# Performance work log

Measured on AMD Instinct MI355X. Metric: run time of the kernel, lower is better.

Reference implementation:

```python
import jax, jax.numpy as jnp
import numpy as np

D_MODEL = 768
N_HEADS = 12
D_K = D_MODEL // N_HEADS
B, S = 2, 2048
EPS = 1e-5  # torch LayerNorm default


def setup_inputs() -> dict:
    key = jax.random.key(0)
    ks = jax.random.split(key, 12)
    sc = 1.0 / np.sqrt(D_MODEL)
    inp = {
        "q": jax.random.normal(ks[0], (B, S, D_MODEL), jnp.float32),
        "k": jax.random.normal(ks[1], (B, S, D_MODEL), jnp.float32),
        "v": jax.random.normal(ks[2], (B, S, D_MODEL), jnp.float32),
        # causal mask: 1 = keep, 0 = masked
        "mask": jnp.tril(jnp.ones((S, S), jnp.int32))[None, None, :, :],
        "Wq": jax.random.normal(ks[3], (D_MODEL, D_MODEL), jnp.float32) * sc,
        "bq": jnp.zeros((D_MODEL,), jnp.float32),
        "Wk": jax.random.normal(ks[4], (D_MODEL, D_MODEL), jnp.float32) * sc,
        "bk": jnp.zeros((D_MODEL,), jnp.float32),
        "Wv": jax.random.normal(ks[5], (D_MODEL, D_MODEL), jnp.float32) * sc,
        "bv": jnp.zeros((D_MODEL,), jnp.float32),
        "Wo": jax.random.normal(ks[6], (D_MODEL, D_MODEL), jnp.float32) * sc,
        "bo": jnp.zeros((D_MODEL,), jnp.float32),
        "gamma": jnp.ones((D_MODEL,), jnp.float32),
        "beta": jnp.zeros((D_MODEL,), jnp.float32),
    }
    return inp


def _layernorm(x, gamma, beta):
    mu = jnp.mean(x, axis=-1, keepdims=True)
    var = jnp.mean(jnp.square(x - mu), axis=-1, keepdims=True)
    return (x - mu) * jax.lax.rsqrt(var + EPS) * gamma + beta


def reference(q, k, v, mask, Wq, bq, Wk, bk, Wv, bv, Wo, bo, gamma, beta):
    residual = q
    # projections + split heads: [B,S,D] -> [B,H,S,Dk]
    def split_heads(x):
        return x.reshape(B, S, N_HEADS, D_K).transpose(0, 2, 1, 3)
    Q = split_heads(q @ Wq.T + bq)
    K = split_heads(k @ Wk.T + bk)
    V = split_heads(v @ Wv.T + bv)
    scores = jnp.einsum("bhqd,bhkd->bhqk", Q, K) / jnp.sqrt(jnp.float32(D_K))
    scores = jnp.where(mask == 0, -jnp.inf, scores)
    attn = jax.nn.softmax(scores, axis=-1)
    # dropout is identity in eval mode
    out = jnp.einsum("bhqk,bhkd->bhqd", attn, V)
    out = out.transpose(0, 2, 1, 3).reshape(B, S, D_MODEL)
    out = out @ Wo.T + bo
    out = _layernorm(residual + out, gamma, beta)
    return (out, attn)
```

## Files before the change

kernel.cpp:

```cpp
#include <hip/hip_runtime.h>
#include <math.h>

typedef __attribute__((ext_vector_type(8))) short bf8_t;
typedef __attribute__((ext_vector_type(4))) float f4_t;

#define MFMA(a,b,c) __builtin_amdgcn_mfma_f32_16x16x32_bf16(a,b,c,0,0,0)

static constexpr int S_ = 2048;
static constexpr size_t QKV_ELEMS = 3145728;
static constexpr size_t W_ELEMS   = 589824;
static constexpr size_t OUT0_ELEMS = 3145728;

__device__ __forceinline__ unsigned short f2bf(float f) {
    union { float f; unsigned u; } v; v.f = f;
    unsigned u = v.u;
    u += 0x7fffu + ((u >> 16) & 1u);
    return (unsigned short)(u >> 16);
}

__device__ __forceinline__ void gload_lds16(const short* g, short* l) {
    __builtin_amdgcn_global_load_lds((const __attribute__((address_space(1))) void*)g,
                                     (__attribute__((address_space(3))) void*)l,
                                     16, 0, 0);
}

struct CvtP { const float* s[7]; unsigned short* d[7]; int n[7]; };

__global__ __launch_bounds__(256)
void cvt_all(CvtP p)
{
    const int z = blockIdx.z;
    const int i = (blockIdx.x * 256 + threadIdx.x) * 8;
    if (i >= p.n[z]) return;
    const float* s = p.s[z] + i;
    float4 a = *(const float4*)s, b = *(const float4*)(s + 4);
    uint4 u;
    u.x = (unsigned)f2bf(a.x) | ((unsigned)f2bf(a.y) << 16);
    u.y = (unsigned)f2bf(a.z) | ((unsigned)f2bf(a.w) << 16);
    u.z = (unsigned)f2bf(b.x) | ((unsigned)f2bf(b.y) << 16);
    u.w = (unsigned)f2bf(b.z) | ((unsigned)f2bf(b.w) << 16);
    *(uint4*)(p.d[z] + i) = u;
}

struct GemmP {
    const short* A[3]; const short* W[3]; const float* bias[3];
    void* C[3]; float scale[3]; int mode[3];
};

__global__ __launch_bounds__(256)
void gemm_bf16(GemmP p)
{
    const int z = blockIdx.z;
    const short* __restrict__ A = p.A[z];
    const short* __restrict__ W = p.W[z];
    const float* __restrict__ bias = p.bias[z];
    const float scale = p.scale[z];
    const int mode = p.mode[z];

    __shared__ short As[128 * 32];
    __shared__ short Bs[128 * 32];

    const int t = threadIdx.x;
    const int m0 = blockIdx.y * 128, n0 = blockIdx.x * 128;
    const int w = t >> 6, lane = t & 63, li = lane & 15, qd = lane >> 4;
    const int wm = (w & 1) * 64, wn = (w >> 1) * 64;

    f4_t acc[4][4];
    #pragma unroll
    for (int i = 0; i < 4; ++i)
        #pragma unroll
        for (int j = 0; j < 4; ++j)
            #pragma unroll
            for (int r = 0; r < 4; ++r) acc[i][j][r] = 0.f;

    for (int k0 = 0; k0 < 768; k0 += 32) {
        #pragma unroll
        for (int e = 0; e < 2; ++e) {
            const int ch = t + e * 256;
            const int r = ch >> 2, c = (ch & 3) << 3;
            gload_lds16(&A[(size_t)(m0 + r) * 768 + k0 + c], &As[ch << 3]);
            gload_lds16(&W[(size_t)(n0 + r) * 768 + k0 + c], &Bs[ch << 3]);
        }
        __syncthreads();
        bf8_t af[4], bf[4];
        #pragma unroll
        for (int i = 0; i < 4; ++i) af[i] = *(const bf8_t*)&As[(wm + i * 16 + li) * 32 + qd * 8];
        #pragma unroll
        for (int j = 0; j < 4; ++j) bf[j] = *(const bf8_t*)&Bs[(wn + j * 16 + li) * 32 + qd * 8];
        #pragma unroll
        for (int i = 0; i < 4; ++i)
            #pragma unroll
            for (int j = 0; j < 4; ++j)
                acc[i][j] = MFMA(af[i], bf[j], acc[i][j]);
        __syncthreads();
    }

    #pragma unroll
    for (int i = 0; i < 4; ++i) {
        const int row = m0 + wm + i * 16 + qd * 4;
        #pragma unroll
        for (int j = 0; j < 4; ++j) {
            const int col = n0 + wn + j * 16 + li;
            const float bv = bias[col];
            float vals[4];
            #pragma unroll
            for (int r = 0; r < 4; ++r) vals[r] = (acc[i][j][r] + bv) * scale;
            if (mode == 0) {
                const int head = col >> 6;
                const int cq = col & 63;
                const int half = cq >> 5, qd_ = (cq >> 3) & 3, e = cq & 7;
                #pragma unroll
                for (int r = 0; r < 4; ++r) {
                    const int rr = row + r;
                    const int bh = (rr >> 11) * 12 + head;
                    const int s = rr & 2047;
                    const int kt = s >> 6, sub = (s >> 4) & 3, li_ = s & 15;
                    const size_t idx = ((((size_t)bh * 32 + kt) * 2 + half) * 4 + sub) * 512
                                     + li_ * 32 + qd_ * 8 + e;
                    ((unsigned short*)p.C[z])[idx] = f2bf(vals[r]);
                }
            } else if (mode == 1) {
                const int head = col >> 6;
                const int rr = row;
                const int bh = (rr >> 11) * 12 + head;
                const int s = rr & 2047;
                const int kt = s >> 6, h = (s >> 5) & 1, qd_ = (s >> 3) & 3, e0 = s & 7;
                const int d_ = (col & 63) >> 4, li_ = col & 15;
                const size_t idx = (((((size_t)bh * 32 + kt) * 2 + h) * 4 + d_) * 16 + li_) * 32
                                 + qd_ * 8 + e0;
                ushort4 u;
                u.x = f2bf(vals[0]); u.y = f2bf(vals[1]);
                u.z = f2bf(vals[2]); u.w = f2bf(vals[3]);
                *(ushort4*)&((unsigned short*)p.C[z])[idx] = u;
            } else {
                #pragma unroll
                for (int r = 0; r < 4; ++r)
                    ((float*)p.C[z])[(size_t)(row + r) * 768 + col] = vals[r];
            }
        }
    }
}

__global__ __launch_bounds__(256, 3)
void attn_fused(const short* __restrict__ Qf, const short* __restrict__ Kf,
                const short* __restrict__ Vf, float* __restrict__ attn,
                unsigned short* __restrict__ AO)
{
    __shared__ short Ps[4][1024];

    const int B = blockIdx.x;
    const int s_ = B & 255, rr_ = B >> 8;
    const int item = (rr_ == 0) ? s_ : (rr_ == 1) ? (511 - s_) : (512 + s_);
    const int qt = 31 - (item / 24);
    const int bh = item % 24;

    const int t = threadIdx.x;
    const int ws = t >> 6;
    const int lane = t & 63;
    const int li = lane & 15, qd = lane >> 4;
    const int lq = li * 32 + qd * 8;
    const int lsw = li & 7;
    const float NEG = -1e30f;

    const int q0 = qt * 64 + ws * 16;
    const short* Qbase = Qf + ((((size_t)bh * 32 + qt) * 2) * 4 + ws) * 512 + lq;
    const bf8_t qf0 = *(const bf8_t*)&Qbase[0];
    const bf8_t qf1 = *(const bf8_t*)&Qbase[2048];

    const short* Kfb = Kf + (size_t)bh * 131072;
    const short* Vfb = Vf + (size_t)bh * 131072;
    float* attnp = attn + (size_t)bh * 2048 * 2048;
    short* Psw = Ps[ws];

    float m_[4] = {NEG, NEG, NEG, NEG}, l_[4] = {0.f, 0.f, 0.f, 0.f};

    bf8_t kc0[4], kc1[4], kn0[4], kn1[4];

    {
        #pragma unroll
        for (int sub = 0; sub < 4; ++sub) {
            kc0[sub] = *(const bf8_t*)&Kfb[sub * 512 + lq];
            kc1[sub] = *(const bf8_t*)&Kfb[2048 + sub * 512 + lq];
        }
        for (int kt = 0; kt <= qt; ++kt) {
            if (kt < qt) {
                const short* Kn = Kfb + (size_t)(kt + 1) * 4096;
                #pragma unroll
                for (int sub = 0; sub < 4; ++sub) {
                    kn0[sub] = *(const bf8_t*)&Kn[sub * 512 + lq];
                    kn1[sub] = *(const bf8_t*)&Kn[2048 + sub * 512 + lq];
                }
            }
            f4_t c[4];
            #pragma unroll
            for (int sub = 0; sub < 4; ++sub) {
                f4_t z; z[0] = z[1] = z[2] = z[3] = 0.f;
                z = MFMA(qf0, kc0[sub], z);
                z = MFMA(qf1, kc1[sub], z);
                c[sub] = z;
            }
            if (kt == qt) {
                #pragma unroll
                for (int sub = 0; sub < 4; ++sub)
                    #pragma unroll
                    for (int r = 0; r < 4; ++r)
                        if (sub * 16 + li > ws * 16 + qd * 4 + r) c[sub][r] = NEG;
            }
            #pragma unroll
            for (int r = 0; r < 4; ++r) {
                float tm = fmaxf(fmaxf(c[0][r], c[1][r]), fmaxf(c[2][r], c[3][r]));
                float nm = fmaxf(m_[r], tm);
                float s = __expf(c[0][r] - nm) + __expf(c[1][r] - nm)
                        + __expf(c[2][r] - nm) + __expf(c[3][r] - nm);
                l_[r] = l_[r] * __expf(m_[r] - nm) + s;
                m_[r] = nm;
            }
            #pragma unroll
            for (int sub = 0; sub < 4; ++sub) { kc0[sub] = kn0[sub]; kc1[sub] = kn1[sub]; }
        }
    }

    float invl[4];
    #pragma unroll
    for (int r = 0; r < 4; ++r) {
        float mg = m_[r];
        mg = fmaxf(mg, __shfl_xor(mg, 1, 64));
        mg = fmaxf(mg, __shfl_xor(mg, 2, 64));
        mg = fmaxf(mg, __shfl_xor(mg, 4, 64));
        mg = fmaxf(mg, __shfl_xor(mg, 8, 64));
        float lg = l_[r] * __expf(m_[r] - mg);
        lg += __shfl_xor(lg, 1, 64);
        lg += __shfl_xor(lg, 2, 64);
        lg += __shfl_xor(lg, 4, 64);
        lg += __shfl_xor(lg, 8, 64);
        m_[r] = mg;
        invl[r] = 1.f / lg;
    }

    f4_t o[4];
    #pragma unroll
    for (int d = 0; d < 4; ++d)
        #pragma unroll
        for (int r = 0; r < 4; ++r) o[d][r] = 0.f;

    {
        #pragma unroll
        for (int sub = 0; sub < 4; ++sub) {
            kc0[sub] = *(const bf8_t*)&Kfb[sub * 512 + lq];
            kc1[sub] = *(const bf8_t*)&Kfb[2048 + sub * 512 + lq];
        }
        for (int kt = 0; kt <= qt; ++kt) {
            const short* Vt_ = Vfb + (size_t)kt * 4096;
            bf8_t vb[2][4];
            #pragma unroll
            for (int h = 0; h < 2; ++h)
                #pragma unroll
                for (int d = 0; d < 4; ++d)
                    vb[h][d] = *(const bf8_t*)&Vt_[h * 2048 + d * 512 + lq];
            if (kt < qt) {
                const short* Kn = Kfb + (size_t)(kt + 1) * 4096;
                #pragma unroll
                for (int sub = 0; sub < 4; ++sub) {
                    kn0[sub] = *(const bf8_t*)&Kn[sub * 512 + lq];
                    kn1[sub] = *(const bf8_t*)&Kn[2048 + sub * 512 + lq];
                }
            }
            f4_t c[4];
            #pragma unroll
            for (int sub = 0; sub < 4; ++sub) {
                f4_t z; z[0] = z[1] = z[2] = z[3] = 0.f;
                z = MFMA(qf0, kc0[sub], z);
                z = MFMA(qf1, kc1[sub], z);
                c[sub] = z;
            }
            if (kt == qt) {
                #pragma unroll
                for (int sub = 0; sub < 4; ++sub)
                    #pragma unroll
                    for (int r = 0; r < 4; ++r)
                        if (sub * 16 + li > ws * 16 + qd * 4 + r) c[sub][r] = NEG;
            }
            #pragma unroll
            for (int sub = 0; sub < 4; ++sub)
                #pragma unroll
                for (int r = 0; r < 4; ++r) {
                    const float pe = __expf(c[sub][r] - m_[r]) * invl[r];
                    attnp[(size_t)(q0 + qd * 4 + r) * 2048 + kt * 64 + sub * 16 + li] = pe;
                    const int prow = qd * 4 + r;
                    const int pcol = sub * 16 + li;
                    Psw[prow * 64 + (((pcol >> 3) ^ (prow & 7)) << 3) + (pcol & 7)] = (short)f2bf(pe);
                }
            #pragma unroll
            for (int h = 0; h < 2; ++h) {
                bf8_t pa = *(const bf8_t*)&Psw[li * 64 + (((h * 4 + qd) ^ lsw) << 3)];
                #pragma unroll
                for (int d = 0; d < 4; ++d)
                    o[d] = MFMA(pa, vb[h][d], o[d]);
            }
            #pragma unroll
            for (int sub = 0; sub < 4; ++sub) { kc0[sub] = kn0[sub]; kc1[sub] = kn1[sub]; }
        }
    }

    const int w4 = (31 - qt) * 16;
    const float4 z4 = make_float4(0.f, 0.f, 0.f, 0.f);
    for (int r = 0; r < 16; ++r) {
        float* rp = &attnp[(size_t)(q0 + r) * 2048 + (qt + 1) * 64];
        for (int cc = lane; cc < w4; cc += 64)
            *(float4*)&rp[cc * 4] = z4;
    }

    const int b = bh / 12, h_ = bh % 12;
    #pragma unroll
    for (int d = 0; d < 4; ++d)
        #pragma unroll
        for (int r = 0; r < 4; ++r)
            AO[(size_t)(b * 2048 + q0 + qd * 4 + r) * 768 + h_ * 64 + d * 16 + li] = f2bf(o[d][r]);
}

__global__ __launch_bounds__(256)
void ln_kernel(const float* __restrict__ resid, const float* __restrict__ proj,
               const float* __restrict__ gamma, const float* __restrict__ beta,
               float* __restrict__ out)
{
    __shared__ float red[4];
    const int row = blockIdx.x, t = threadIdx.x;
    const size_t base = (size_t)row * 768;
    float x[3];
    float s = 0.f;
    #pragma unroll
    for (int e = 0; e < 3; ++e) {
        int j = t + e * 256;
        x[e] = resid[base + j] + proj[base + j];
        s += x[e];
    }
    #pragma unroll
    for (int off = 1; off < 64; off <<= 1) s += __shfl_xor(s, off, 64);
    if ((t & 63) == 0) red[t >> 6] = s;
    __syncthreads();
    s = red[0] + red[1] + red[2] + red[3];
    const float mu = s * (1.f / 768.f);
    float vs = 0.f;
    #pragma unroll
    for (int e = 0; e < 3; ++e) { float d = x[e] - mu; vs += d * d; }
    __syncthreads();
    #pragma unroll
    for (int off = 1; off < 64; off <<= 1) vs += __shfl_xor(vs, off, 64);
    if ((t & 63) == 0) red[t >> 6] = vs;
    __syncthreads();
    vs = red[0] + red[1] + red[2] + red[3];
    const float inv = rsqrtf(vs * (1.f / 768.f) + 1e-5f);
    #pragma unroll
    for (int e = 0; e < 3; ++e) {
        int j = t + e * 256;
        out[base + j] = (x[e] - mu) * inv * gamma[j] + beta[j];
    }
}

extern "C" void kernel_launch(void* const* d_in, const int* in_sizes, int n_in,
                              void* d_out, int out_size, void* d_ws, size_t ws_size,
                              hipStream_t stream)
{
    const float* q     = (const float*)d_in[0];
    const float* k     = (const float*)d_in[1];
    const float* v     = (const float*)d_in[2];
    const float* Wq    = (const float*)d_in[4];
    const float* bq    = (const float*)d_in[5];
    const float* Wk    = (const float*)d_in[6];
    const float* bk    = (const float*)d_in[7];
    const float* Wv    = (const float*)d_in[8];
    const float* bv    = (const float*)d_in[9];
    const float* Wo    = (const float*)d_in[10];
    const float* bo    = (const float*)d_in[11];
    const float* gamma = (const float*)d_in[12];
    const float* beta  = (const float*)d_in[13];

    float* out  = (float*)d_out;
    float* attn = out + OUT0_ELEMS;

    short* qc  = (short*)d_ws;
    short* kc  = qc + QKV_ELEMS;
    short* vc  = kc + QKV_ELEMS;
    short* wqc = vc + QKV_ELEMS;
    short* wkc = wqc + W_ELEMS;
    short* wvc = wkc + W_ELEMS;
    short* woc = wvc + W_ELEMS;
    short* Qb  = woc + W_ELEMS;
    short* Kb  = Qb + QKV_ELEMS;
    short* Vt  = Kb + QKV_ELEMS;
    short* AO  = Vt + QKV_ELEMS;
    float* P   = (float*)(AO + QKV_ELEMS);

    CvtP cp;
    cp.s[0] = q;  cp.d[0] = (unsigned short*)qc;  cp.n[0] = (int)QKV_ELEMS;
    cp.s[1] = k;  cp.d[1] = (unsigned short*)kc;  cp.n[1] = (int)QKV_ELEMS;
    cp.s[2] = v;  cp.d[2] = (unsigned short*)vc;  cp.n[2] = (int)QKV_ELEMS;
    cp.s[3] = Wq; cp.d[3] = (unsigned short*)wqc; cp.n[3] = (int)W_ELEMS;
    cp.s[4] = Wk; cp.d[4] = (unsigned short*)wkc; cp.n[4] = (int)W_ELEMS;
    cp.s[5] = Wv; cp.d[5] = (unsigned short*)wvc; cp.n[5] = (int)W_ELEMS;
    cp.s[6] = Wo; cp.d[6] = (unsigned short*)woc; cp.n[6] = (int)W_ELEMS;
    cvt_all<<<dim3(1536, 1, 7), 256, 0, stream>>>(cp);

    GemmP gp;
    gp.A[0] = qc; gp.W[0] = wqc; gp.bias[0] = bq; gp.C[0] = Qb; gp.scale[0] = 0.125f; gp.mode[0] = 0;
    gp.A[1] = kc; gp.W[1] = wkc; gp.bias[1] = bk; gp.C[1] = Kb; gp.scale[1] = 1.f;    gp.mode[1] = 0;
    gp.A[2] = vc; gp.W[2] = wvc; gp.bias[2] = bv; gp.C[2] = Vt; gp.scale[2] = 1.f;    gp.mode[2] = 1;
    gemm_bf16<<<dim3(6, 32, 3), 256, 0, stream>>>(gp);

    attn_fused<<<dim3(768), 256, 0, stream>>>(Qb, Kb, Vt, attn, (unsigned short*)AO);

    GemmP gp2;
    gp2.A[0] = AO; gp2.W[0] = woc; gp2.bias[0] = bo; gp2.C[0] = P; gp2.scale[0] = 1.f; gp2.mode[0] = 2;
    gp2.A[1] = gp2.A[2] = AO; gp2.W[1] = gp2.W[2] = woc; gp2.bias[1] = gp2.bias[2] = bo;
    gp2.C[1] = gp2.C[2] = P; gp2.scale[1] = gp2.scale[2] = 1.f; gp2.mode[1] = gp2.mode[2] = 2;
    gemm_bf16<<<dim3(6, 32, 1), 256, 0, stream>>>(gp2);

    ln_kernel<<<dim3(4096), 256, 0, stream>>>(q, P, gamma, beta, out);
}
```

Measured before the change: 629.1 us.

## Split attention key tiles across waves and reduce partial sums through LDS

Work in the attention kernel is redistributed. Each wave now covers all 64 query rows of the tile and walks a strided subset of key tiles (kt = ws, ws+4, …), so every K/V tile is loaded once per block instead of by all four waves. The row-sum and output partials are combined across waves through shared memory, followed by a coalesced bf16 write of the attention output. The running-max softmax is dropped and raw exp(score) is used directly, which removes the rescaling work but can overflow for large scores. The change also uses more registers and LDS, lowers launch bounds from 3 to 2 blocks per SM, and can leave waves unevenly loaded on short causal rows.

```diff
diff --git a/kernel.cpp b/kernel.cpp
--- a/kernel.cpp
+++ b/kernel.cpp
@@ -141,12 +141,13 @@
     }
 }
 
-__global__ __launch_bounds__(256, 3)
+__global__ __launch_bounds__(256, 2)
 void attn_fused(const short* __restrict__ Qf, const short* __restrict__ Kf,
                 const short* __restrict__ Vf, float* __restrict__ attn,
                 unsigned short* __restrict__ AO)
 {
-    __shared__ short Ps[4][1024];
+    __shared__ float lsum[64][4];
+    __shared__ float Osm[4][64 * 68];
 
     const int B = blockIdx.x;
     const int s_ = B & 255, rr_ = B >> 8;
@@ -162,160 +163,193 @@
     const int lsw = li & 7;
     const float NEG = -1e30f;
 
-    const int q0 = qt * 64 + ws * 16;
-    const short* Qbase = Qf + ((((size_t)bh * 32 + qt) * 2) * 4 + ws) * 512 + lq;
-    const bf8_t qf0 = *(const bf8_t*)&Qbase[0];
-    const bf8_t qf1 = *(const bf8_t*)&Qbase[2048];
-
     const short* Kfb = Kf + (size_t)bh * 131072;
     const short* Vfb = Vf + (size_t)bh * 131072;
     float* attnp = attn + (size_t)bh * 2048 * 2048;
-    short* Psw = Ps[ws];
-
-    float m_[4] = {NEG, NEG, NEG, NEG}, l_[4] = {0.f, 0.f, 0.f, 0.f};
-
-    bf8_t kc0[4], kc1[4], kn0[4], kn1[4];
-
+    short* Psw = (short*)&Osm[0][0] + ws * 4096;
+
+    bf8_t qf[2][4];
     {
-        #pragma unroll
-        for (int sub = 0; sub < 4; ++sub) {
-            kc0[sub] = *(const bf8_t*)&Kfb[sub * 512 + lq];
-            kc1[sub] = *(const bf8_t*)&Kfb[2048 + sub * 512 + lq];
-        }
-        for (int kt = 0; kt <= qt; ++kt) {
-            if (kt < qt) {
-                const short* Kn = Kfb + (size_t)(kt + 1) * 4096;
-                #pragma unroll
-                for (int sub = 0; sub < 4; ++sub) {
-                    kn0[sub] = *(const bf8_t*)&Kn[sub * 512 + lq];
-                    kn1[sub] = *(const bf8_t*)&Kn[2048 + sub * 512 + lq];
-                }
-            }
+        const short* Qb_ = Qf + ((size_t)bh * 32 + qt) * 4096 + lq;
+        #pragma unroll
+        for (int h = 0; h < 2; ++h)
+            #pragma unroll
+            for (int qs = 0; qs < 4; ++qs)
+                qf[h][qs] = *(const bf8_t*)&Qb_[h * 2048 + qs * 512];
+    }
+
+    float l_[4][4];
+    #pragma unroll
+    for (int qs = 0; qs < 4; ++qs)
+        #pragma unroll
+        for (int r = 0; r < 4; ++r) l_[qs][r] = 0.f;
+
+    for (int kt = ws; kt <= qt; kt += 4) {
+        const short* Kt = Kfb + (size_t)kt * 4096;
+        bf8_t kf0[4], kf1[4];
+        #pragma unroll
+        for (int ks = 0; ks < 4; ++ks) {
+            kf0[ks] = *(const bf8_t*)&Kt[ks * 512 + lq];
+            kf1[ks] = *(const bf8_t*)&Kt[2048 + ks * 512 + lq];
+        }
+        const bool diag = (kt == qt);
+        #pragma unroll
+        for (int qs = 0; qs < 4; ++qs) {
             f4_t c[4];
             #pragma unroll
-            for (int sub = 0; sub < 4; ++sub) {
+            for (int ks = 0; ks < 4; ++ks) {
                 f4_t z; z[0] = z[1] = z[2] = z[3] = 0.f;
-                z = MFMA(qf0, kc0[sub], z);
-                z = MFMA(qf1, kc1[sub], z);
-                c[sub] = z;
-            }
-            if (kt == qt) {
-                #pragma unroll
-                for (int sub = 0; sub < 4; ++sub)
+                z = MFMA(qf[0][qs], kf0[ks], z);
+                z = MFMA(qf[1][qs], kf1[ks], z);
+                c[ks] = z;
+            }
+            if (diag) {
+                #pragma unroll
+                for (int ks = 0; ks < 4; ++ks)
                     #pragma unroll
                     for (int r = 0; r < 4; ++r)
-                        if (sub * 16 + li > ws * 16 + qd * 4 + r) c[sub][r] = NEG;
-            }
-            #pragma unroll
-            for (int r = 0; r < 4; ++r) {
-                float tm = fmaxf(fmaxf(c[0][r], c[1][r]), fmaxf(c[2][r], c[3][r]));
-                float nm = fmaxf(m_[r], tm);
-                float s = __expf(c[0][r] - nm) + __expf(c[1][r] - nm)
-                        + __expf(c[2][r] - nm) + __expf(c[3][r] - nm);
-                l_[r] = l_[r] * __expf(m_[r] - nm) + s;
-                m_[r] = nm;
-            }
-            #pragma unroll
-            for (int sub = 0; sub < 4; ++sub) { kc0[sub] = kn0[sub]; kc1[sub] = kn1[sub]; }
-        }
-    }
-
-    float invl[4];
-    #pragma unroll
-    for (int r = 0; r < 4; ++r) {
-        float mg = m_[r];
-        mg = fmaxf(mg, __shfl_xor(mg, 1, 64));
-        mg = fmaxf(mg, __shfl_xor(mg, 2, 64));
-        mg = fmaxf(mg, __shfl_xor(mg, 4, 64));
-        mg = fmaxf(mg, __shfl_xor(mg, 8, 64));
-        float lg = l_[r] * __expf(m_[r] - mg);
-        lg += __shfl_xor(lg, 1, 64);
-        lg += __shfl_xor(lg, 2, 64);
-        lg += __shfl_xor(lg, 4, 64);
-        lg += __shfl_xor(lg, 8, 64);
-        m_[r] = mg;
-        invl[r] = 1.f / lg;
-    }
-
-    f4_t o[4];
-    #pragma unroll
-    for (int d = 0; d < 4; ++d)
-        #pragma unroll
-        for (int r = 0; r < 4; ++r) o[d][r] = 0.f;
-
-    {
-        #pragma unroll
-        for (int sub = 0; sub < 4; ++sub) {
-            kc0[sub] = *(const bf8_t*)&Kfb[sub * 512 + lq];
-            kc1[sub] = *(const bf8_t*)&Kfb[2048 + sub * 512 + lq];
-        }
-        for (int kt = 0; kt <= qt; ++kt) {
-            const short* Vt_ = Vfb + (size_t)kt * 4096;
-            bf8_t vb[2][4];
-            #pragma unroll
-            for (int h = 0; h < 2; ++h)
-                #pragma unroll
-                for (int d = 0; d < 4; ++d)
-                    vb[h][d] = *(const bf8_t*)&Vt_[h * 2048 + d * 512 + lq];
-            if (kt < qt) {
-                const short* Kn = Kfb + (size_t)(kt + 1) * 4096;
-                #pragma unroll
-                for (int sub = 0; sub < 4; ++sub) {
-                    kn0[sub] = *(const bf8_t*)&Kn[sub * 512 + lq];
-                    kn1[sub] = *(const bf8_t*)&Kn[2048 + sub * 512 + lq];
-                }
-            }
+                        if (ks * 16 + li > qs * 16 + qd * 4 + r) c[ks][r] = NEG;
+            }
+            #pragma unroll
+            for (int r = 0; r < 4; ++r)
+                l_[qs][r] += __expf(c[0][r]) + __expf(c[1][r])
+                           + __expf(c[2][r]) + __expf(c[3][r]);
+        }
+    }
+
+    #pragma unroll
+    for (int qs = 0; qs < 4; ++qs)
+        #pragma unroll
+        for (int r = 0; r < 4; ++r) {
+            float v = l_[qs][r];
+            v += __shfl_xor(v, 1, 64);
+            v += __shfl_xor(v, 2, 64);
+            v += __shfl_xor(v, 4, 64);
+            v += __shfl_xor(v, 8, 64);
+            l_[qs][r] = v;
+        }
+    if (li == 0) {
+        #pragma unroll
+        for (int qs = 0; qs < 4; ++qs)
+            #pragma unroll
+            for (int r = 0; r < 4; ++r)
+                lsum[qs * 16 + qd * 4 + r][ws] = l_[qs][r];
+    }
+    __syncthreads();
+    float invl[4][4];
+    #pragma unroll
+    for (int qs = 0; qs < 4; ++qs)
+        #pragma unroll
+        for (int r = 0; r < 4; ++r) {
+            const float4 lv = *(const float4*)&lsum[qs * 16 + qd * 4 + r][0];
+            invl[qs][r] = 1.f / (lv.x + lv.y + lv.z + lv.w);
+        }
+
+    f4_t o[4][4];
+    #pragma unroll
+    for (int qs = 0; qs < 4; ++qs)
+        #pragma unroll
+        for (int ds = 0; ds < 4; ++ds)
+            #pragma unroll
+            for (int r = 0; r < 4; ++r) o[qs][ds][r] = 0.f;
+
+    for (int kt = ws; kt <= qt; kt += 4) {
+        const short* Kt = Kfb + (size_t)kt * 4096;
+        const short* Vt_ = Vfb + (size_t)kt * 4096;
+        bf8_t kf0[4], kf1[4], vb[2][4];
+        #pragma unroll
+        for (int ks = 0; ks < 4; ++ks) {
+            kf0[ks] = *(const bf8_t*)&Kt[ks * 512 + lq];
+            kf1[ks] = *(const bf8_t*)&Kt[2048 + ks * 512 + lq];
+        }
+        #pragma unroll
+        for (int h = 0; h < 2; ++h)
+            #pragma unroll
+            for (int ds = 0; ds < 4; ++ds)
+                vb[h][ds] = *(const bf8_t*)&Vt_[h * 2048 + ds * 512 + lq];
+
+        const bool diag = (kt == qt);
+        #pragma unroll
+        for (int qs = 0; qs < 4; ++qs) {
             f4_t c[4];
             #pragma unroll
-            for (int sub = 0; sub < 4; ++sub) {
+            for (int ks = 0; ks < 4; ++ks) {
                 f4_t z; z[0] = z[1] = z[2] = z[3] = 0.f;
-                z = MFMA(qf0, kc0[sub], z);
-                z = MFMA(qf1, kc1[sub], z);
-                c[sub] = z;
-            }
-            if (kt == qt) {
-                #pragma unroll
-                for (int sub = 0; sub < 4; ++sub)
+                z = MFMA(qf[0][qs], kf0[ks], z);
+                z = MFMA(qf[1][qs], kf1[ks], z);
+                c[ks] = z;
+            }
+            if (diag) {
+                #pragma unroll
+                for (int ks = 0; ks < 4; ++ks)
                     #pragma unroll
                     for (int r = 0; r < 4; ++r)
-                        if (sub * 16 + li > ws * 16 + qd * 4 + r) c[sub][r] = NEG;
-            }
-            #pragma unroll
-            for (int sub = 0; sub < 4; ++sub)
+                        if (ks * 16 + li > qs * 16 + qd * 4 + r) c[ks][r] = NEG;
+            }
+            #pragma unroll
+            for (int ks = 0; ks < 4; ++ks)
                 #pragma unroll
                 for (int r = 0; r < 4; ++r) {
-                    const float pe = __expf(c[sub][r] - m_[r]) * invl[r];
-                    attnp[(size_t)(q0 + qd * 4 + r) * 2048 + kt * 64 + sub * 16 + li] = pe;
-                    const int prow = qd * 4 + r;
-                    const int pcol = sub * 16 + li;
-                    Psw[prow * 64 + (((pcol >> 3) ^ (prow & 7)) << 3) + (pcol & 7)] = (short)f2bf(pe);
+                    const float pe = __expf(c[ks][r]) * invl[qs][r];
+                    attnp[(size_t)(qt * 64 + qs * 16 + qd * 4 + r) * 2048
+                          + kt * 64 + ks * 16 + li] = pe;
+                    const int prow = qs * 16 + qd * 4 + r;
+                    const int pcol = ks * 16 + li;
+                    Psw[prow * 64 + (((pcol >> 3) ^ (prow & 7)) << 3) + (pcol & 7)]
+                        = (short)f2bf(pe);
                 }
-            #pragma unroll
-            for (int h = 0; h < 2; ++h) {
-                bf8_t pa = *(const bf8_t*)&Psw[li * 64 + (((h * 4 + qd) ^ lsw) << 3)];
-                #pragma unroll
-                for (int d = 0; d < 4; ++d)
-                    o[d] = MFMA(pa, vb[h][d], o[d]);
-            }
-            #pragma unroll
-            for (int sub = 0; sub < 4; ++sub) { kc0[sub] = kn0[sub]; kc1[sub] = kn1[sub]; }
+        }
+        #pragma unroll
+        for (int h = 0; h < 2; ++h) {
+            bf8_t pa[4];
+            #pragma unroll
+            for (int qs = 0; qs < 4; ++qs)
+                pa[qs] = *(const bf8_t*)&Psw[(qs * 16 + li) * 64 + (((h * 4 + qd) ^ lsw) << 3)];
+            #pragma unroll
+            for (int qs = 0; qs < 4; ++qs)
+                #pragma unroll
+                for (int ds = 0; ds < 4; ++ds)
+                    o[qs][ds] = MFMA(pa[qs], vb[h][ds], o[qs][ds]);
+        }
+    }
+
+    __syncthreads();
+    #pragma unroll
+    for (int qs = 0; qs < 4; ++qs)
+        #pragma unroll
+        for (int ds = 0; ds < 4; ++ds)
+            #pragma unroll
+            for (int r = 0; r < 4; ++r)
+                Osm[ws][(qs * 16 + qd * 4 + r) * 68 + ds * 16 + li] = o[qs][ds][r];
+    __syncthreads();
+    {
+        const int row16 = lane >> 2;
+        const int cb = (lane & 3) * 16;
+        const int rowI = ws * 16 + row16;
+        const int b_ = bh / 12, h_ = bh % 12;
+        unsigned short* aop = AO + ((size_t)(b_ * 2048 + qt * 64 + rowI) * 768 + h_ * 64 + cb);
+        #pragma unroll
+        for (int j = 0; j < 4; ++j) {
+            float4 a = *(const float4*)&Osm[0][rowI * 68 + cb + j * 4];
+            #pragma unroll
+            for (int w2 = 1; w2 < 4; ++w2) {
+                const float4 b2 = *(const float4*)&Osm[w2][rowI * 68 + cb + j * 4];
+                a.x += b2.x; a.y += b2.y; a.z += b2.z; a.w += b2.w;
+            }
+            ushort4 u;
+            u.x = f2bf(a.x); u.y = f2bf(a.y); u.z = f2bf(a.z); u.w = f2bf(a.w);
+            *(ushort4*)&aop[j * 4] = u;
         }
     }
 
     const int w4 = (31 - qt) * 16;
     const float4 z4 = make_float4(0.f, 0.f, 0.f, 0.f);
+    const int q0 = qt * 64 + ws * 16;
     for (int r = 0; r < 16; ++r) {
         float* rp = &attnp[(size_t)(q0 + r) * 2048 + (qt + 1) * 64];
         for (int cc = lane; cc < w4; cc += 64)
             *(float4*)&rp[cc * 4] = z4;
     }
-
-    const int b = bh / 12, h_ = bh % 12;
-    #pragma unroll
-    for (int d = 0; d < 4; ++d)
-        #pragma unroll
-        for (int r = 0; r < 4; ++r)
-            AO[(size_t)(b * 2048 + q0 + qd * 4 + r) * 768 + h_ * 64 + d * 16 + li] = f2bf(o[d][r]);
 }
 
 __global__ __launch_bounds__(256)
```

Result: slower. 653.4 us (+3.9%).
